# Performance work log

Measured on AMD Instinct MI355X. Metric: run time of the kernel, lower is better.

## Reference

```python
import jax, jax.numpy as jnp
import numpy as np

C_CT, C_MRI, C_OUT = 64, 64, 64
B, D, H, W = 1, 8, 32, 32


def setup_inputs() -> dict:
    key = jax.random.key(0)
    ks = jax.random.split(key, 18)
    s = 0.05
    inp = {
        "ct_features": jax.random.normal(ks[0], (B, C_CT, D, H, W), jnp.float32),
        "mri_features": jax.random.normal(ks[1], (B, C_MRI, D, H, W), jnp.float32),
        # 1x1x1 Conv3d == per-voxel linear: weight (out, in), bias (out,)
        "wq_ct": jax.random.normal(ks[2], (C_OUT, C_CT), jnp.float32) * s,
        "bq_ct": jax.random.normal(ks[3], (C_OUT,), jnp.float32) * s,
        "wk_mri": jax.random.normal(ks[4], (C_OUT, C_MRI), jnp.float32) * s,
        "bk_mri": jax.random.normal(ks[5], (C_OUT,), jnp.float32) * s,
        "wv_mri": jax.random.normal(ks[6], (C_OUT, C_MRI), jnp.float32) * s,
        "bv_mri": jax.random.normal(ks[7], (C_OUT,), jnp.float32) * s,
        "wq_mri": jax.random.normal(ks[8], (C_OUT, C_MRI), jnp.float32) * s,
        "bq_mri": jax.random.normal(ks[9], (C_OUT,), jnp.float32) * s,
        "wk_ct": jax.random.normal(ks[10], (C_OUT, C_CT), jnp.float32) * s,
        "bk_ct": jax.random.normal(ks[11], (C_OUT,), jnp.float32) * s,
        "wv_ct": jax.random.normal(ks[12], (C_OUT, C_CT), jnp.float32) * s,
        "bv_ct": jax.random.normal(ks[13], (C_OUT,), jnp.float32) * s,
        "wo": jax.random.normal(ks[14], (C_OUT, 2 * C_OUT), jnp.float32) * s,
        "bo": jax.random.normal(ks[15], (C_OUT,), jnp.float32) * s,
    }
    return inp


def _proj(x_flat, w, b):
    # x_flat: (B, Cin, N); 1x1x1 conv -> (B, Cout, N)
    return jnp.einsum("oc,bcn->bon", w, x_flat) + b[None, :, None]


def _forward(ct, mri, wq_ct, bq_ct, wk_mri, bk_mri, wv_mri, bv_mri,
             wq_mri, bq_mri, wk_ct, bk_ct, wv_ct, bv_ct, wo, bo):
    b, _, d, h, w = ct.shape
    n = d * h * w
    ct_f = ct.reshape(b, ct.shape[1], n)
    mri_f = mri.reshape(b, mri.shape[1], n)
    scale = 1.0 / np.sqrt(C_OUT).astype(np.float32)

    # CT queries attend over MRI keys/values
    ct_q = _proj(ct_f, wq_ct, bq_ct)      # (B, C, N)
    mri_k = _proj(mri_f, wk_mri, bk_mri)  # (B, C, N)
    mri_v = _proj(mri_f, wv_mri, bv_mri)  # (B, C, N)
    attn_ct = jax.nn.softmax(jnp.einsum("bci,bcj->bij", ct_q, mri_k) * scale, axis=-1)
    ct_att = jnp.einsum("bcj,bij->bci", mri_v, attn_ct)  # (B, C, N)

    # MRI queries attend over CT keys/values
    mri_q = _proj(mri_f, wq_mri, bq_mri)
    ct_k = _proj(ct_f, wk_ct, bk_ct)
    ct_v = _proj(ct_f, wv_ct, bv_ct)
    attn_mri = jax.nn.softmax(jnp.einsum("bci,bcj->bij", mri_q, ct_k) * scale, axis=-1)
    mri_att = jnp.einsum("bcj,bij->bci", ct_v, attn_mri)

    fused = jnp.concatenate([ct_att, mri_att], axis=1)  # (B, 2C, N)
    out = _proj(fused, wo, bo)  # (B, C, N)
    return out.reshape(b, C_OUT, d, h, w)


def reference(ct_features, mri_features, wq_ct, bq_ct, wk_mri, bk_mri,
              wv_mri, bv_mri, wq_mri, bq_mri, wk_ct, bk_ct, wv_ct, bv_ct,
              wo, bo):
    return _forward(ct_features, mri_features, wq_ct, bq_ct, wk_mri, bk_mri,
                    wv_mri, bv_mri, wq_mri, bq_mri, wk_ct, bk_ct,
                    wv_ct, bv_ct, wo, bo)
```

## Files before the change

### kernel.cpp

```cpp
#include <hip/hip_runtime.h>
#include <stdint.h>

constexpr int N = 8192;
constexpr float QSCALE = 0.18033688011112042f;
constexpr int SPLIT = 4;

typedef __attribute__((ext_vector_type(4))) float f32x4;
typedef __attribute__((ext_vector_type(4))) unsigned int u32x4;
typedef __attribute__((ext_vector_type(2))) unsigned int u32x2;
typedef __attribute__((ext_vector_type(4))) unsigned short u16x4;

__device__ inline unsigned short f2bf(float f) {
  unsigned u = __builtin_bit_cast(unsigned, f);
  u += 0x7FFFu + ((u >> 16) & 1u);
  return (unsigned short)(u >> 16);
}
__device__ inline float bf2f(unsigned short u) {
  return __builtin_bit_cast(float, (unsigned)u << 16);
}
__device__ inline unsigned cvtpk(float a, float b) {
  unsigned r;
  asm("v_cvt_pk_bf16_f32 %0, %1, %2" : "=v"(r) : "v"(a), "v"(b));
  return r;
}

__device__ inline void mfma16x16x32bf16(f32x4& d, u32x4 a, u32x4 b) {
  asm volatile("v_mfma_f32_16x16x32_bf16 %0, %1, %2, %0" : "+v"(d) : "v"(a), "v"(b));
}
__device__ inline void mfma_guard() {
  __builtin_amdgcn_sched_barrier(0);
  asm volatile("s_nop 7\n\ts_nop 7");
  __builtin_amdgcn_sched_barrier(0);
}
__device__ inline void gload16(const void* src, void* lds) {
  __builtin_amdgcn_global_load_lds(
      (const __attribute__((address_space(1))) unsigned int*)src,
      (__attribute__((address_space(3))) unsigned int*)lds, 16, 0, 0);
}

struct ProjArgs {
  const float* x[6];
  const float* w[6];
  const float* b[6];
  unsigned short* o[6];
  int mode[6];
  float scale[6];
};

__global__ __launch_bounds__(256) void proj_kernel(ProjArgs A) {
  const int p = blockIdx.y;
  const float* __restrict__ x = A.x[p];
  const float* __restrict__ w = A.w[p];
  const float* __restrict__ bias = A.b[p];
  unsigned short* __restrict__ out = A.o[p];
  const int n0 = blockIdx.x * 64;
  __shared__ float Xs[64][64];
  __shared__ float Ws[64][64];
  const int t = threadIdx.x;
#pragma unroll
  for (int i = 0; i < 4; i++) {
    int s = t + i * 256;
    ((u32x4*)Ws)[s] = ((const u32x4*)w)[s];
  }
#pragma unroll
  for (int i = 0; i < 4; i++) {
    int s = t + i * 256;
    int c = s >> 4, nc = s & 15;
    *(u32x4*)&Xs[c][nc * 4] = *(const u32x4*)&x[c * N + n0 + nc * 4];
  }
  __syncthreads();
  const int n = t & 63, h = t >> 6;
  float acc[16];
#pragma unroll
  for (int o = 0; o < 16; o++) acc[o] = bias[h * 16 + o];
  for (int c = 0; c < 64; c++) {
    float xv = Xs[c][n];
#pragma unroll
    for (int o = 0; o < 16; o++) acc[o] = fmaf(Ws[h * 16 + o][c], xv, acc[o]);
  }
  const float sc = A.scale[p];
  if (A.mode[p] == 0) {
    unsigned short* po = out + (size_t)(n0 + n) * 64 + h * 16;
#pragma unroll
    for (int o = 0; o < 16; o++) po[o] = f2bf(acc[o] * sc);
  } else {
#pragma unroll
    for (int o = 0; o < 16; o++) out[(size_t)(h * 16 + o) * N + n0 + n] = f2bf(acc[o] * sc);
  }
}

__global__ __launch_bounds__(256, 2) void attn_kernel(
    const unsigned short* __restrict__ Q0, const unsigned short* __restrict__ K0,
    const unsigned short* __restrict__ V0, const unsigned short* __restrict__ Q1,
    const unsigned short* __restrict__ K1, const unsigned short* __restrict__ V1,
    unsigned short* __restrict__ Opart, float* __restrict__ Lsum) {
  const int bid = blockIdx.x;
  const int slice = bid & 7;
  const int qb = bid >> 3;
  const int dir = slice >> 2;
  const int chunk = slice & 3;
  const unsigned short* __restrict__ Q = dir ? Q1 : Q0;
  const unsigned short* __restrict__ K = dir ? K1 : K0;
  const unsigned short* __restrict__ V = dir ? V1 : V0;

  __shared__ char smem[74752];

  const int t = threadIdx.x;
  const int lane = t & 63, w = t >> 6;
  const int g = lane >> 4, sl = lane & 15;
  char* const pw = smem + 65536 + w * 2304;
  const int kvbase = chunk * 2048;

  const int srowoff = lane >> 3;
  const int kswz = ((lane & 7) ^ (lane >> 3)) * 16;
  const int vchsub = lane >> 4;
  const int vc16 = lane & 15;
  const char* const Kc = (const char*)K;
  const char* const Vc = (const char*)V;

#define STAGE(jtile, slot)                                                     \
  do {                                                                         \
    const int j0s = kvbase + (jtile) * 128;                                    \
    _Pragma("unroll") for (int i = 0; i < 4; i++) {                            \
      const int krow = (w * 4 + i) * 8 + srowoff;                              \
      gload16(Kc + (size_t)(j0s + krow) * 128 + kswz,                          \
              smem + (slot) * 16384 + (w * 4 + i) * 1024);                     \
      const int vch = (w * 4 + i) * 4 + vchsub;                                \
      gload16(Vc + (size_t)vch * (N * 2) + (size_t)j0s * 2 +                   \
                  ((vc16 ^ (vch & 7)) * 16),                                   \
              smem + 32768 + (slot) * 16384 + (w * 4 + i) * 1024);             \
    }                                                                          \
  } while (0)

  u32x4 qf[2][2];
#pragma unroll
  for (int rb = 0; rb < 2; rb++) {
    const int qrow = qb * 128 + w * 32 + rb * 16 + sl;
#pragma unroll
    for (int ks = 0; ks < 2; ks++)
      qf[rb][ks] = *(const u32x4*)(Q + (size_t)qrow * 64 + ks * 32 + 8 * g);
  }

  f32x4 acc[4][2];
#pragma unroll
  for (int mb = 0; mb < 4; mb++)
#pragma unroll
    for (int rb = 0; rb < 2; rb++)
#pragma unroll
      for (int r = 0; r < 4; r++) acc[mb][rb][r] = 0.f;
  float lpart[2] = {0.f, 0.f};

  STAGE(0, 0);
  for (int jt = 0; jt < 16; ++jt) {
    asm volatile("s_waitcnt vmcnt(0)" ::: "memory");
    __builtin_amdgcn_s_barrier();
    __builtin_amdgcn_sched_barrier(0);
    const int cur = jt & 1;
    if (jt + 1 < 16) STAGE(jt + 1, cur ^ 1);
    char* const Kl = smem + cur * 16384;
    char* const Vl = smem + 32768 + cur * 16384;

    f32x4 st[2][4][2];
#pragma unroll
    for (int h = 0; h < 2; h++) {
      u32x4 kf[4][2];
#pragma unroll
      for (int jb = 0; jb < 4; jb++) {
        const int row = h * 64 + jb * 16 + sl;
        const int rs = (row & 7) << 4;
#pragma unroll
        for (int ks = 0; ks < 2; ks++)
          kf[jb][ks] = *(const u32x4*)(Kl + row * 128 + ((ks * 64 + 16 * g) ^ rs));
      }
      __builtin_amdgcn_s_setprio(1);
#pragma unroll
      for (int jb = 0; jb < 4; jb++)
#pragma unroll
        for (int rb = 0; rb < 2; rb++) {
#pragma unroll
          for (int r = 0; r < 4; r++) st[h][jb][rb][r] = 0.f;
          mfma16x16x32bf16(st[h][jb][rb], kf[jb][0], qf[rb][0]);
          mfma16x16x32bf16(st[h][jb][rb], kf[jb][1], qf[rb][1]);
        }
      __builtin_amdgcn_s_setprio(0);
    }

#pragma unroll
    for (int h = 0; h < 2; h++) {
      u32x4 vf[4][2];
#pragma unroll
      for (int mb = 0; mb < 4; mb++) {
        const int row = mb * 16 + sl;
        const int rs = (row & 7) << 4;
#pragma unroll
        for (int ks = 0; ks < 2; ks++)
          vf[mb][ks] = *(const u32x4*)(Vl + row * 256 +
                                       ((h * 128 + ks * 64 + 16 * g) ^ rs));
      }
#pragma unroll
      for (int rb = 0; rb < 2; rb++) {
#pragma unroll
        for (int jb = 0; jb < 4; jb++) {
          float e0 = __builtin_amdgcn_exp2f(st[h][jb][rb][0]);
          float e1 = __builtin_amdgcn_exp2f(st[h][jb][rb][1]);
          float e2 = __builtin_amdgcn_exp2f(st[h][jb][rb][2]);
          float e3 = __builtin_amdgcn_exp2f(st[h][jb][rb][3]);
          lpart[rb] += (e0 + e1) + (e2 + e3);
          u32x2 pk;
          pk[0] = cvtpk(e0, e1);
          pk[1] = cvtpk(e2, e3);
          *(u32x2*)(pw + sl * 144 + jb * 32 + 8 * g) = pk;
        }
        u32x4 pf0 = *(const u32x4*)(pw + sl * 144 + 16 * g);
        u32x4 pf1 = *(const u32x4*)(pw + sl * 144 + 64 + 16 * g);
        __builtin_amdgcn_s_setprio(1);
#pragma unroll
        for (int mb = 0; mb < 4; mb++) {
          mfma16x16x32bf16(acc[mb][rb], vf[mb][0], pf0);
          mfma16x16x32bf16(acc[mb][rb], vf[mb][1], pf1);
        }
        __builtin_amdgcn_s_setprio(0);
      }
    }
  }
#undef STAGE
  mfma_guard();

#pragma unroll
  for (int rb = 0; rb < 2; rb++) {
    lpart[rb] += __shfl_xor(lpart[rb], 16);
    lpart[rb] += __shfl_xor(lpart[rb], 32);
  }

#pragma unroll
  for (int rb = 0; rb < 2; rb++) {
    const int q = rb * 16 + sl;
    const int qg = qb * 128 + w * 32 + q;
    const size_t pbase = ((size_t)slice * N + qg) * 64;
#pragma unroll
    for (int mb = 0; mb < 4; mb++) {
      u32x2 pk;
      pk[0] = cvtpk(acc[mb][rb][0], acc[mb][rb][1]);
      pk[1] = cvtpk(acc[mb][rb][2], acc[mb][rb][3]);
      *(u32x2*)(Opart + pbase + mb * 16 + 4 * g) = pk;
    }
    if (g == 0) Lsum[(size_t)slice * N + qg] = lpart[rb];
  }
}

__global__ __launch_bounds__(256) void oproj_kernel(
    const unsigned short* __restrict__ Opart, const float* __restrict__ Lsum,
    const float* __restrict__ wo, const float* __restrict__ bo,
    float* __restrict__ out) {
  __shared__ float Fs[128][32];
  __shared__ float Ws[64][128];
  const int t = threadIdx.x;
  const int n0 = blockIdx.x * 32;
#pragma unroll
  for (int i = 0; i < 8; i++) {
    int s = t + i * 256;
    ((u32x4*)Ws)[s] = ((const u32x4*)wo)[s];
  }
  const int q = t & 31;
  const int cg = t >> 5;
#pragma unroll
  for (int dir = 0; dir < 2; dir++) {
    float lt = 0.f;
#pragma unroll
    for (int c = 0; c < 4; c++) lt += Lsum[(size_t)(dir * SPLIT + c) * N + n0 + q];
    const float rD = 1.0f / lt;
#pragma unroll
    for (int i = 0; i < 2; i++) {
      const int ch4 = cg * 2 + i;
      float s0 = 0.f, s1 = 0.f, s2 = 0.f, s3 = 0.f;
#pragma unroll
      for (int c = 0; c < 4; c++) {
        u16x4 v = *(const u16x4*)(Opart +
            ((size_t)(dir * SPLIT + c) * N + n0 + q) * 64 + ch4 * 4);
        s0 += bf2f(v[0]); s1 += bf2f(v[1]); s2 += bf2f(v[2]); s3 += bf2f(v[3]);
      }
      Fs[dir * 64 + ch4 * 4 + 0][q] = s0 * rD;
      Fs[dir * 64 + ch4 * 4 + 1][q] = s1 * rD;
      Fs[dir * 64 + ch4 * 4 + 2][q] = s2 * rD;
      Fs[dir * 64 + ch4 * 4 + 3][q] = s3 * rD;
    }
  }
  __syncthreads();
  const int n = t & 31, h = t >> 5;
  float acc[8];
#pragma unroll
  for (int o = 0; o < 8; o++) acc[o] = bo[h * 8 + o];
  for (int ch = 0; ch < 128; ch++) {
    float fv = Fs[ch][n];
#pragma unroll
    for (int o = 0; o < 8; o++) acc[o] = fmaf(Ws[h * 8 + o][ch], fv, acc[o]);
  }
#pragma unroll
  for (int o = 0; o < 8; o++) out[(size_t)(h * 8 + o) * N + n0 + n] = acc[o];
}

extern "C" void kernel_launch(void* const* d_in, const int* in_sizes, int n_in,
                              void* d_out, int out_size, void* d_ws, size_t ws_size,
                              hipStream_t stream) {
  const float* ct     = (const float*)d_in[0];
  const float* mri    = (const float*)d_in[1];
  const float* wq_ct  = (const float*)d_in[2];
  const float* bq_ct  = (const float*)d_in[3];
  const float* wk_mri = (const float*)d_in[4];
  const float* bk_mri = (const float*)d_in[5];
  const float* wv_mri = (const float*)d_in[6];
  const float* bv_mri = (const float*)d_in[7];
  const float* wq_mri = (const float*)d_in[8];
  const float* bq_mri = (const float*)d_in[9];
  const float* wk_ct  = (const float*)d_in[10];
  const float* bk_ct  = (const float*)d_in[11];
  const float* wv_ct  = (const float*)d_in[12];
  const float* bv_ct  = (const float*)d_in[13];
  const float* wo     = (const float*)d_in[14];
  const float* bo     = (const float*)d_in[15];

  char* ws = (char*)d_ws;
  const size_t MB = (size_t)1 << 20;
  unsigned short* Qt_ct  = (unsigned short*)(ws + 0 * MB);
  unsigned short* Kt_mri = (unsigned short*)(ws + 1 * MB);
  unsigned short* V_mri  = (unsigned short*)(ws + 2 * MB);
  unsigned short* Qt_mri = (unsigned short*)(ws + 3 * MB);
  unsigned short* Kt_ct  = (unsigned short*)(ws + 4 * MB);
  unsigned short* V_ct   = (unsigned short*)(ws + 5 * MB);
  unsigned short* Opart  = (unsigned short*)(ws + 6 * MB);
  float* Lsum            = (float*)(ws + 14 * MB);

  ProjArgs A;
  A.x[0] = ct;  A.w[0] = wq_ct;  A.b[0] = bq_ct;  A.o[0] = Qt_ct;  A.mode[0] = 0; A.scale[0] = QSCALE;
  A.x[1] = mri; A.w[1] = wk_mri; A.b[1] = bk_mri; A.o[1] = Kt_mri; A.mode[1] = 0; A.scale[1] = 1.f;
  A.x[2] = mri; A.w[2] = wv_mri; A.b[2] = bv_mri; A.o[2] = V_mri;  A.mode[2] = 1; A.scale[2] = 1.f;
  A.x[3] = mri; A.w[3] = wq_mri; A.b[3] = bq_mri; A.o[3] = Qt_mri; A.mode[3] = 0; A.scale[3] = QSCALE;
  A.x[4] = ct;  A.w[4] = wk_ct;  A.b[4] = bk_ct;  A.o[4] = Kt_ct;  A.mode[4] = 0; A.scale[4] = 1.f;
  A.x[5] = ct;  A.w[5] = wv_ct;  A.b[5] = bv_ct;  A.o[5] = V_ct;   A.mode[5] = 1; A.scale[5] = 1.f;

  proj_kernel<<<dim3(128, 6), 256, 0, stream>>>(A);
  attn_kernel<<<dim3(512), 256, 0, stream>>>(Qt_ct, Kt_mri, V_mri,
                                             Qt_mri, Kt_ct, V_ct, Opart, Lsum);
  oproj_kernel<<<dim3(256), 256, 0, stream>>>(Opart, Lsum, wo, bo, (float*)d_out);
}
```

Measured before the change: 72.66 us.

## Halve KV tile to 64 and raise attention occupancy to three blocks per CU

The attention kernel now stages 64 keys per iteration instead of 128, doubling the iteration count while cutting the double-buffered K/V shared memory from 64KB to 32KB and total LDS to 48KB. Launch bounds are raised to 3 blocks per SM, and the P scratch buffer is laid out per row-block with an XOR swizzle instead of padding. The aim is higher occupancy so memory latency and exp work can overlap across waves. In exchange there are more barriers per key, tighter register limits, and possible spills.

```diff
diff --git a/kernel.cpp b/kernel.cpp
--- a/kernel.cpp
+++ b/kernel.cpp
@@ -89,7 +89,7 @@
   }
 }
 
-__global__ __launch_bounds__(256, 2) void attn_kernel(
+__global__ __launch_bounds__(256, 3) void attn_kernel(
     const unsigned short* __restrict__ Q0, const unsigned short* __restrict__ K0,
     const unsigned short* __restrict__ V0, const unsigned short* __restrict__ Q1,
     const unsigned short* __restrict__ K1, const unsigned short* __restrict__ V1,
@@ -103,32 +103,29 @@
   const unsigned short* __restrict__ K = dir ? K1 : K0;
   const unsigned short* __restrict__ V = dir ? V1 : V0;
 
-  __shared__ char smem[74752];
+  __shared__ char smem[49152];
 
   const int t = threadIdx.x;
   const int lane = t & 63, w = t >> 6;
   const int g = lane >> 4, sl = lane & 15;
-  char* const pw = smem + 65536 + w * 2304;
+  char* const pw = smem + 32768 + w * 4096;
   const int kvbase = chunk * 2048;
+  const int qswz = (sl & 7) << 4;
 
   const int srowoff = lane >> 3;
-  const int kswz = ((lane & 7) ^ (lane >> 3)) * 16;
-  const int vchsub = lane >> 4;
-  const int vc16 = lane & 15;
+  const int swzb = ((lane & 7) ^ (lane >> 3)) * 16;
   const char* const Kc = (const char*)K;
   const char* const Vc = (const char*)V;
 
 #define STAGE(jtile, slot)                                                     \
   do {                                                                         \
-    const int j0s = kvbase + (jtile) * 128;                                    \
-    _Pragma("unroll") for (int i = 0; i < 4; i++) {                            \
-      const int krow = (w * 4 + i) * 8 + srowoff;                              \
-      gload16(Kc + (size_t)(j0s + krow) * 128 + kswz,                          \
-              smem + (slot) * 16384 + (w * 4 + i) * 1024);                     \
-      const int vch = (w * 4 + i) * 4 + vchsub;                                \
-      gload16(Vc + (size_t)vch * (N * 2) + (size_t)j0s * 2 +                   \
-                  ((vc16 ^ (vch & 7)) * 16),                                   \
-              smem + 32768 + (slot) * 16384 + (w * 4 + i) * 1024);             \
+    const int j0s = kvbase + (jtile) * 64;                                     \
+    _Pragma("unroll") for (int i = 0; i < 2; i++) {                            \
+      const int row = (w * 2 + i) * 8 + srowoff;                               \
+      gload16(Kc + (size_t)(j0s + row) * 128 + swzb,                           \
+              smem + (slot) * 8192 + (w * 2 + i) * 1024);                      \
+      gload16(Vc + (size_t)row * (N * 2) + (size_t)j0s * 2 + swzb,             \
+              smem + 16384 + (slot) * 8192 + (w * 2 + i) * 1024);              \
     }                                                                          \
   } while (0)
 
@@ -151,76 +148,76 @@
   float lpart[2] = {0.f, 0.f};
 
   STAGE(0, 0);
-  for (int jt = 0; jt < 16; ++jt) {
+  for (int jt = 0; jt < 32; ++jt) {
     asm volatile("s_waitcnt vmcnt(0)" ::: "memory");
     __builtin_amdgcn_s_barrier();
     __builtin_amdgcn_sched_barrier(0);
     const int cur = jt & 1;
-    if (jt + 1 < 16) STAGE(jt + 1, cur ^ 1);
-    char* const Kl = smem + cur * 16384;
-    char* const Vl = smem + 32768 + cur * 16384;
-
-    f32x4 st[2][4][2];
-#pragma unroll
-    for (int h = 0; h < 2; h++) {
-      u32x4 kf[4][2];
+    if (jt + 1 < 32) STAGE(jt + 1, cur ^ 1);
+    char* const Kl = smem + cur * 8192;
+    char* const Vl = smem + 16384 + cur * 8192;
+
+    u32x4 kf[4][2];
+#pragma unroll
+    for (int jb = 0; jb < 4; jb++) {
+      const int row = jb * 16 + sl;
+      const int rs = (row & 7) << 4;
+#pragma unroll
+      for (int ks = 0; ks < 2; ks++)
+        kf[jb][ks] = *(const u32x4*)(Kl + row * 128 + ((ks * 64 + 16 * g) ^ rs));
+    }
+
+    f32x4 st[4][2];
+    __builtin_amdgcn_s_setprio(1);
+#pragma unroll
+    for (int jb = 0; jb < 4; jb++)
+#pragma unroll
+      for (int rb = 0; rb < 2; rb++) {
+#pragma unroll
+        for (int r = 0; r < 4; r++) st[jb][rb][r] = 0.f;
+        mfma16x16x32bf16(st[jb][rb], kf[jb][0], qf[rb][0]);
+        mfma16x16x32bf16(st[jb][rb], kf[jb][1], qf[rb][1]);
+      }
+    __builtin_amdgcn_s_setprio(0);
+    mfma_guard();
+
+    u32x4 vf[4][2];
+#pragma unroll
+    for (int mb = 0; mb < 4; mb++) {
+      const int row = mb * 16 + sl;
+      const int rs = (row & 7) << 4;
+#pragma unroll
+      for (int ks = 0; ks < 2; ks++)
+        vf[mb][ks] = *(const u32x4*)(Vl + row * 128 + ((ks * 64 + 16 * g) ^ rs));
+    }
+
+#pragma unroll
+    for (int rb = 0; rb < 2; rb++) {
 #pragma unroll
       for (int jb = 0; jb < 4; jb++) {
-        const int row = h * 64 + jb * 16 + sl;
-        const int rs = (row & 7) << 4;
-#pragma unroll
-        for (int ks = 0; ks < 2; ks++)
-          kf[jb][ks] = *(const u32x4*)(Kl + row * 128 + ((ks * 64 + 16 * g) ^ rs));
+        float e0 = __builtin_amdgcn_exp2f(st[jb][rb][0]);
+        float e1 = __builtin_amdgcn_exp2f(st[jb][rb][1]);
+        float e2 = __builtin_amdgcn_exp2f(st[jb][rb][2]);
+        float e3 = __builtin_amdgcn_exp2f(st[jb][rb][3]);
+        lpart[rb] += (e0 + e1) + (e2 + e3);
+        u32x2 pk;
+        pk[0] = cvtpk(e0, e1);
+        pk[1] = cvtpk(e2, e3);
+        *(u32x2*)(pw + rb * 2048 + sl * 128 + ((jb * 32 + 8 * g) ^ qswz)) = pk;
       }
+    }
+
+#pragma unroll
+    for (int rb = 0; rb < 2; rb++) {
+      u32x4 pf0 = *(const u32x4*)(pw + rb * 2048 + sl * 128 + ((16 * g) ^ qswz));
+      u32x4 pf1 = *(const u32x4*)(pw + rb * 2048 + sl * 128 + ((64 + 16 * g) ^ qswz));
       __builtin_amdgcn_s_setprio(1);
 #pragma unroll
-      for (int jb = 0; jb < 4; jb++)
-#pragma unroll
-        for (int rb = 0; rb < 2; rb++) {
-#pragma unroll
-          for (int r = 0; r < 4; r++) st[h][jb][rb][r] = 0.f;
-          mfma16x16x32bf16(st[h][jb][rb], kf[jb][0], qf[rb][0]);
-          mfma16x16x32bf16(st[h][jb][rb], kf[jb][1], qf[rb][1]);
-        }
+      for (int mb = 0; mb < 4; mb++) {
+        mfma16x16x32bf16(acc[mb][rb], vf[mb][0], pf0);
+        mfma16x16x32bf16(acc[mb][rb], vf[mb][1], pf1);
+      }
       __builtin_amdgcn_s_setprio(0);
-    }
-
-#pragma unroll
-    for (int h = 0; h < 2; h++) {
-      u32x4 vf[4][2];
-#pragma unroll
-      for (int mb = 0; mb < 4; mb++) {
-        const int row = mb * 16 + sl;
-        const int rs = (row & 7) << 4;
-#pragma unroll
-        for (int ks = 0; ks < 2; ks++)
-          vf[mb][ks] = *(const u32x4*)(Vl + row * 256 +
-                                       ((h * 128 + ks * 64 + 16 * g) ^ rs));
-      }
-#pragma unroll
-      for (int rb = 0; rb < 2; rb++) {
-#pragma unroll
-        for (int jb = 0; jb < 4; jb++) {
-          float e0 = __builtin_amdgcn_exp2f(st[h][jb][rb][0]);
-          float e1 = __builtin_amdgcn_exp2f(st[h][jb][rb][1]);
-          float e2 = __builtin_amdgcn_exp2f(st[h][jb][rb][2]);
-          float e3 = __builtin_amdgcn_exp2f(st[h][jb][rb][3]);
-          lpart[rb] += (e0 + e1) + (e2 + e3);
-          u32x2 pk;
-          pk[0] = cvtpk(e0, e1);
-          pk[1] = cvtpk(e2, e3);
-          *(u32x2*)(pw + sl * 144 + jb * 32 + 8 * g) = pk;
-        }
-        u32x4 pf0 = *(const u32x4*)(pw + sl * 144 + 16 * g);
-        u32x4 pf1 = *(const u32x4*)(pw + sl * 144 + 64 + 16 * g);
-        __builtin_amdgcn_s_setprio(1);
-#pragma unroll
-        for (int mb = 0; mb < 4; mb++) {
-          mfma16x16x32bf16(acc[mb][rb], vf[mb][0], pf0);
-          mfma16x16x32bf16(acc[mb][rb], vf[mb][1], pf1);
-        }
-        __builtin_amdgcn_s_setprio(0);
-      }
     }
   }
 #undef STAGE
```

Measured after the change: 73.05 us. About the same (+0.5%).
